# Performance work log

Hardware: AMD Instinct MI355X
Metric: run time of the kernel (lower is better)

The kernel has to match this reference:

```python
import jax, jax.numpy as jnp
import numpy as np

NEG = -1e30  # safe stand-in for -inf in fp32


def _seg_logsumexp(scores, seg, num_segments):
    m = jax.ops.segment_max(scores, seg, num_segments=num_segments)
    m = jnp.maximum(m, NEG)
    s = jax.ops.segment_sum(jnp.exp(scores - m[seg]), seg, num_segments=num_segments)
    return jnp.where(s > 0, m + jnp.log(s), NEG)


def _chain_ll(x, length, src, dst, pdf, logw, init_lp, final_lp):
    # Log-domain HMM forward recursion over an edge-list graph.
    # x: [T, D] log-likelihoods; returns scalar log total path weight.
    S = init_lp.shape[0]
    T = x.shape[0]

    def step(alpha, inputs):
        xt, t = inputs
        scores = alpha[src] + logw + xt[pdf]          # [E]
        new_alpha = _seg_logsumexp(scores, dst, S)    # [S]
        alpha = jnp.where(t < length, new_alpha, alpha)
        return alpha, None

    alpha, _ = jax.lax.scan(step, init_lp, (x, jnp.arange(T)))
    return jax.nn.logsumexp(alpha + final_lp)


def chain_loss(x, x_lengths, den_src, den_dst, den_pdf, den_logw, den_init, den_final,
               num_src, num_dst, num_pdf, num_logw, num_init, num_final):
    # Denominator: one shared graph for all batch elements.
    den_ll = jax.vmap(_chain_ll, in_axes=(0, 0, None, None, None, None, None, None))(
        x, x_lengths, den_src, den_dst, den_pdf, den_logw, den_init, den_final)
    # Numerator: one graph per utterance.
    num_ll = jax.vmap(_chain_ll)(
        x, x_lengths, num_src, num_dst, num_pdf, num_logw, num_init, num_final)
    den_objf = jnp.sum(den_ll)
    num_objf = jnp.sum(num_ll)
    objf = -(num_objf - den_objf)
    return objf / jnp.sum(x_lengths).astype(x.dtype)  # avg=True


def setup_inputs() -> dict:
    key = jax.random.key(0)
    ks = jax.random.split(key, 16)
    B, T, D = 32, 500, 3072
    S_den, E_den = 4000, 120000
    S_num, E_num = 200, 600

    x = jax.random.normal(ks[0], (B, T, D), dtype=jnp.float32)
    x_lengths = jnp.sort(jax.random.randint(ks[1], (B,), T // 2, T + 1, dtype=jnp.int32))[::-1]

    den_src = jax.random.randint(ks[2], (E_den,), 0, S_den, dtype=jnp.int32)
    den_dst = jax.random.randint(ks[3], (E_den,), 0, S_den, dtype=jnp.int32)
    den_pdf = jax.random.randint(ks[4], (E_den,), 0, D, dtype=jnp.int32)
    den_logw = -5.0 * jax.random.uniform(ks[5], (E_den,), dtype=jnp.float32)
    den_init = -3.0 * jax.random.uniform(ks[6], (S_den,), dtype=jnp.float32)
    den_final = -3.0 * jax.random.uniform(ks[7], (S_den,), dtype=jnp.float32)

    num_src = jax.random.randint(ks[8], (B, E_num), 0, S_num, dtype=jnp.int32)
    num_dst = jax.random.randint(ks[9], (B, E_num), 0, S_num, dtype=jnp.int32)
    num_pdf = jax.random.randint(ks[10], (B, E_num), 0, D, dtype=jnp.int32)
    num_logw = -5.0 * jax.random.uniform(ks[11], (B, E_num), dtype=jnp.float32)
    num_init = -3.0 * jax.random.uniform(ks[12], (B, S_num), dtype=jnp.float32)
    num_final = -3.0 * jax.random.uniform(ks[13], (B, S_num), dtype=jnp.float32)

    return {"x": x, "x_lengths": x_lengths,
            "den_src": den_src, "den_dst": den_dst, "den_pdf": den_pdf,
            "den_logw": den_logw, "den_init": den_init, "den_final": den_final,
            "num_src": num_src, "num_dst": num_dst, "num_pdf": num_pdf,
            "num_logw": num_logw, "num_init": num_init, "num_final": num_final}


def reference(x, x_lengths, den_src, den_dst, den_pdf, den_logw, den_init, den_final,
              num_src, num_dst, num_pdf, num_logw, num_init, num_final):
    return chain_loss(x, x_lengths, den_src, den_dst, den_pdf, den_logw, den_init, den_final,
                      num_src, num_dst, num_pdf, num_logw, num_init, num_final)
```

## Files before the change

### kernel.cpp

```cpp
#include <hip/hip_runtime.h>

constexpr int B_     = 32;
constexpr int T_     = 500;
constexpr int D_     = 3072;
constexpr int S_DEN  = 4000;
constexpr int E_DEN  = 120000;
constexpr int S_NUM  = 200;
constexpr int E_NUM  = 600;
constexpr int NCHUNK = 8;
constexpr int WTGT   = (E_DEN + 2 * E_NUM) / NCHUNK;
constexpr int ECAP   = 15488;
constexpr int NTB    = 512;

__global__ void zero_ints(int* p, int n) {
    int i = blockIdx.x * 256 + threadIdx.x;
    if (i < n) p[i] = 0;
}

__global__ void hist_den(const int* __restrict__ dst, int* __restrict__ cnt) {
    int e = blockIdx.x * 256 + threadIdx.x;
    if (e < E_DEN) atomicAdd(&cnt[dst[e]], 1);
}

__global__ void hist_num(const int* __restrict__ dst, int* __restrict__ cnt) {
    int b = blockIdx.y, j = blockIdx.x * 256 + threadIdx.x;
    if (j < E_NUM) atomicAdd(&cnt[b * S_NUM + dst[b * E_NUM + j]], 1);
}

__global__ void scan_den(int* __restrict__ cnt_cur, int* __restrict__ row) {
    __shared__ int part[1024];
    int tid = threadIdx.x, base = tid * 4;
    int c[4], pre[4], s = 0;
    #pragma unroll
    for (int j = 0; j < 4; ++j) {
        int idx = base + j;
        c[j] = (idx < S_DEN) ? cnt_cur[idx] : 0;
        pre[j] = s; s += c[j];
    }
    part[tid] = s; __syncthreads();
    for (int off = 1; off < 1024; off <<= 1) {
        int v = (tid >= off) ? part[tid - off] : 0; __syncthreads();
        part[tid] += v; __syncthreads();
    }
    int offs = (tid > 0) ? part[tid - 1] : 0;
    #pragma unroll
    for (int j = 0; j < 4; ++j) {
        int idx = base + j;
        if (idx < S_DEN) { row[idx] = offs + pre[j]; cnt_cur[idx] = offs + pre[j]; }
    }
    if (tid == 1023) row[S_DEN] = part[1023];
}

__global__ void scan_num(int* __restrict__ cnt_cur, int* __restrict__ row) {
    __shared__ int part[256];
    int b = blockIdx.x, tid = threadIdx.x;
    int c = (tid < S_NUM) ? cnt_cur[b * S_NUM + tid] : 0;
    part[tid] = c; __syncthreads();
    for (int off = 1; off < 256; off <<= 1) {
        int v = (tid >= off) ? part[tid - off] : 0; __syncthreads();
        part[tid] += v; __syncthreads();
    }
    int excl = part[tid] - c;
    if (tid < S_NUM) { row[b * (S_NUM + 1) + tid] = excl; cnt_cur[b * S_NUM + tid] = excl; }
    if (tid == 255) row[b * (S_NUM + 1) + S_NUM] = part[255];
}

__global__ void scatter_den(const int* __restrict__ src, const int* __restrict__ dst,
                            const int* __restrict__ pdf, const float* __restrict__ logw,
                            int* __restrict__ cur, int2* __restrict__ csr) {
    int e = blockIdx.x * 256 + threadIdx.x;
    if (e >= E_DEN) return;
    int pos = atomicAdd(&cur[dst[e]], 1);
    csr[pos] = make_int2(src[e] | (pdf[e] << 12), __float_as_int(__expf(logw[e])));
}

__global__ void scatter_num(const int* __restrict__ src, const int* __restrict__ dst,
                            const int* __restrict__ pdf, const float* __restrict__ logw,
                            int* __restrict__ cur, int2* __restrict__ csr) {
    int b = blockIdx.y, j = blockIdx.x * 256 + threadIdx.x;
    if (j >= E_NUM) return;
    int e = b * E_NUM + j;
    int pos = atomicAdd(&cur[b * S_NUM + dst[e]], 1);
    csr[b * E_NUM + pos] = make_int2(src[e] | (pdf[e] << 12), __float_as_int(__expf(logw[e])));
}

__global__ void part_den(const int* __restrict__ row, int* __restrict__ part) {
    int r = threadIdx.x;
    if (r > NCHUNK) return;
    if (r == 0)        { part[0] = 0; return; }
    if (r == NCHUNK)   { part[NCHUNK] = S_DEN; return; }
    int target = r * WTGT; if (target > E_DEN) target = E_DEN;
    int lo = 0, hi = S_DEN;
    while (lo < hi) { int mid = (lo + hi) >> 1; if (row[mid] < target) lo = mid + 1; else hi = mid; }
    part[r] = lo;
}

__global__ __launch_bounds__(NTB, 1)
void chain_persist(const float* __restrict__ x, const int* __restrict__ x_lengths,
                   const int* __restrict__ den_row, const int2* __restrict__ den_csr,
                   const int* __restrict__ part,
                   const int* __restrict__ num_row, const int2* __restrict__ num_csr,
                   const float* __restrict__ den_init, const float* __restrict__ den_final,
                   const float* __restrict__ num_init, const float* __restrict__ num_final,
                   unsigned long long* __restrict__ EAslot,
                   unsigned long long* __restrict__ Fflag,
                   float* __restrict__ ll) {
    __shared__ int2   csr_d[ECAP];
    __shared__ float4 ex4[D_ / 4];
    __shared__ float  eal[S_DEN];
    __shared__ int2   csr_n[E_NUM];
    __shared__ float  eal_n[S_NUM];
    __shared__ float  red[8], red_n[8];
    float* ex = (float*)ex4;

    const int tid = threadIdx.x;
    const int b   = blockIdx.x & 31;
    const int r   = blockIdx.x >> 5;
    const int len = x_lengths[b];

    const int s0 = part[r], s1 = part[r + 1];
    const int e0 = den_row[s0], e1 = den_row[s1];
    const int ne = e1 - e0;
    for (int i = tid; i < ne; i += NTB) csr_d[i] = den_csr[e0 + i];
    const int sa = s0 + tid, sb = s0 + tid + NTB;
    int ba = 0, eaA = 0, bb = 0, ebB = 0;
    if (sa < s1) { ba = den_row[sa] - e0; eaA = den_row[sa + 1] - e0; }
    if (sb < s1) { bb = den_row[sb] - e0; ebB = den_row[sb + 1] - e0; }
    for (int s = tid; s < S_DEN; s += NTB) eal[s] = __expf(den_init[s]);

    int nb = 0, neE = 0;
    if (r == NCHUNK - 1) {
        for (int i = tid; i < E_NUM; i += NTB) csr_n[i] = num_csr[b * E_NUM + i];
        if (tid < S_NUM) {
            nb  = num_row[b * (S_NUM + 1) + tid];
            neE = num_row[b * (S_NUM + 1) + tid + 1];
            eal_n[tid] = __expf(num_init[b * S_NUM + tid]);
        }
    }

    const float* xb = x + (size_t)b * T_ * D_;
    const bool  has2 = tid < (D_ / 4 - NTB);
    float4 xr0, xr1;
    {
        const float4* p = (const float4*)xb;
        xr0 = p[tid];
        xr1 = has2 ? p[tid + NTB] : make_float4(0.f, 0.f, 0.f, 0.f);
        float4 ev;
        ev.x = __expf(fminf(xr0.x, 60.f)); ev.y = __expf(fminf(xr0.y, 60.f));
        ev.z = __expf(fminf(xr0.z, 60.f)); ev.w = __expf(fminf(xr0.w, 60.f));
        ex4[tid] = ev;
        if (has2) {
            float4 e1v;
            e1v.x = __expf(fminf(xr1.x, 60.f)); e1v.y = __expf(fminf(xr1.y, 60.f));
            e1v.z = __expf(fminf(xr1.z, 60.f)); e1v.w = __expf(fminf(xr1.w, 60.f));
            ex4[tid + NTB] = e1v;
        }
        if (len > 1) {
            const float4* pn = (const float4*)(xb + (size_t)D_);
            xr0 = pn[tid];
            if (has2) xr1 = pn[tid + NTB];
        }
    }
    __syncthreads();

    float off = 0.f, offn = 0.f, acc0 = 0.f, acc1 = 0.f, accn = 0.f;
    float inv_prev = 1.f;

    for (int t = 0; t < len; ++t) {
        float raw0 = 0.f, raw1 = 0.f;
        if (sa < s1) {
            float a0 = 0.f, a1 = 0.f;
            int e = ba;
            for (; e + 2 <= eaA; e += 2) {
                int2 p0 = csr_d[e], p1 = csr_d[e + 1];
                a0 += eal[p0.x & 0xFFF] * __int_as_float(p0.y) * ex[p0.x >> 12];
                a1 += eal[p1.x & 0xFFF] * __int_as_float(p1.y) * ex[p1.x >> 12];
            }
            if (e < eaA) {
                int2 p0 = csr_d[e];
                a0 += eal[p0.x & 0xFFF] * __int_as_float(p0.y) * ex[p0.x >> 12];
            }
            raw0 = a0 + a1;
        }
        if (sb < s1) {
            float a0 = 0.f, a1 = 0.f;
            int e = bb;
            for (; e + 2 <= ebB; e += 2) {
                int2 p0 = csr_d[e], p1 = csr_d[e + 1];
                a0 += eal[p0.x & 0xFFF] * __int_as_float(p0.y) * ex[p0.x >> 12];
                a1 += eal[p1.x & 0xFFF] * __int_as_float(p1.y) * ex[p1.x >> 12];
            }
            if (e < ebB) {
                int2 p0 = csr_d[e];
                a0 += eal[p0.x & 0xFFF] * __int_as_float(p0.y) * ex[p0.x >> 12];
            }
            raw1 = a0 + a1;
        }
        acc0 = raw0 * inv_prev;
        acc1 = raw1 * inv_prev;

        if (t + 1 < len) {
            unsigned long long* slw = EAslot + ((size_t)(t & 1) * B_ + b) * S_DEN;
            const unsigned long long tg = (unsigned long long)(unsigned)(t + 1) << 32;
            if (sa < s1)
                __hip_atomic_store(&slw[sa], tg | __float_as_uint(acc0),
                                   __ATOMIC_RELAXED, __HIP_MEMORY_SCOPE_AGENT);
            if (sb < s1)
                __hip_atomic_store(&slw[sb], tg | __float_as_uint(acc1),
                                   __ATOMIC_RELAXED, __HIP_MEMORY_SCOPE_AGENT);
        }

        float lmax_n = 0.f;
        if (r == NCHUNK - 1) {
            if (tid < S_NUM) {
                float a = 0.f;
                for (int e = nb; e < neE; ++e) {
                    int2 p0 = csr_n[e];
                    a += eal_n[p0.x & 0xFFF] * __int_as_float(p0.y) * ex[p0.x >> 12];
                }
                accn = a; lmax_n = a;
            }
            #pragma unroll
            for (int o = 32; o > 0; o >>= 1) lmax_n = fmaxf(lmax_n, __shfl_down(lmax_n, o));
            if ((tid & 63) == 0) red_n[tid >> 6] = lmax_n;
        }
        __syncthreads();

        if (r == NCHUNK - 1) {
            float Mn = red_n[0];
            #pragma unroll
            for (int w = 1; w < 8; ++w) Mn = fmaxf(Mn, red_n[w]);
            if (!(Mn > 0.f)) Mn = 1.f;
            if (tid < S_NUM) eal_n[tid] = accn / Mn;
            offn += __logf(Mn);
        }

        if (t + 1 < len) {
            float4 ev;
            ev.x = __expf(fminf(xr0.x, 60.f)); ev.y = __expf(fminf(xr0.y, 60.f));
            ev.z = __expf(fminf(xr0.z, 60.f)); ev.w = __expf(fminf(xr0.w, 60.f));
            ex4[tid] = ev;
            if (has2) {
                float4 e1v;
                e1v.x = __expf(fminf(xr1.x, 60.f)); e1v.y = __expf(fminf(xr1.y, 60.f));
                e1v.z = __expf(fminf(xr1.z, 60.f)); e1v.w = __expf(fminf(xr1.w, 60.f));
                ex4[tid + NTB] = e1v;
            }
            if (t + 2 < len) {
                const float4* pn = (const float4*)(xb + (size_t)(t + 2) * D_);
                xr0 = pn[tid];
                if (has2) xr1 = pn[tid + NTB];
            }

            const unsigned long long* slr = EAslot + ((size_t)(t & 1) * B_ + b) * S_DEN;
            const unsigned want = (unsigned)(t + 1);
            float mv = 0.f;
            unsigned rdy = 0;
            while (rdy != 0xFFu) {
                #pragma unroll
                for (int k = 0; k < 8; ++k) {
                    if (rdy & (1u << k)) continue;
                    int s = tid + k * NTB;
                    if (s >= S_DEN) { rdy |= 1u << k; continue; }
                    unsigned long long v = __hip_atomic_load(&slr[s],
                                             __ATOMIC_RELAXED, __HIP_MEMORY_SCOPE_AGENT);
                    if ((unsigned)(v >> 32) == want) {
                        float f = __uint_as_float((unsigned)v);
                        eal[s] = f;
                        mv = fmaxf(mv, f);
                        rdy |= 1u << k;
                    }
                }
                if (rdy != 0xFFu) __builtin_amdgcn_s_sleep(1);
            }
            #pragma unroll
            for (int o = 32; o > 0; o >>= 1) mv = fmaxf(mv, __shfl_down(mv, o));
            if ((tid & 63) == 0) red[tid >> 6] = mv;
            __syncthreads();

            float M = red[0];
            #pragma unroll
            for (int w = 1; w < 8; ++w) M = fmaxf(M, red[w]);
            if (!(M > 0.f)) M = 1.f;
            off += __logf(M);
            inv_prev = 1.f / M;
        }
    }

    float fs = 0.f;
    if (sa < s1) fs += acc0 * __expf(den_final[sa]);
    if (sb < s1) fs += acc1 * __expf(den_final[sb]);
    #pragma unroll
    for (int o = 32; o > 0; o >>= 1) fs += __shfl_down(fs, o);
    if ((tid & 63) == 0) red[tid >> 6] = fs;
    __syncthreads();

    if (tid == 0) {
        float bf = 0.f;
        #pragma unroll
        for (int w = 0; w < 8; ++w) bf += red[w];
        unsigned long long pv = ((unsigned long long)(unsigned)len << 32) |
                                (unsigned long long)__float_as_uint(bf);
        __hip_atomic_store(&Fflag[b * 8 + r], pv, __ATOMIC_RELAXED, __HIP_MEMORY_SCOPE_AGENT);
    }

    if (r == 0 && tid < 64) {
        float sv = 0.f;
        bool rdy = (tid >= 8);
        const unsigned want = (unsigned)len;
        while (true) {
            if (!rdy) {
                unsigned long long v = __hip_atomic_load(&Fflag[b * 8 + tid],
                                         __ATOMIC_RELAXED, __HIP_MEMORY_SCOPE_AGENT);
                if ((unsigned)(v >> 32) == want) { rdy = true; sv = __uint_as_float((unsigned)v); }
            }
            if (__all(rdy)) break;
            __builtin_amdgcn_s_sleep(1);
        }
        #pragma unroll
        for (int o = 4; o > 0; o >>= 1) sv += __shfl_down(sv, o);
        if (tid == 0) ll[b] = __logf(sv) + off;
    }

    if (r == NCHUNK - 1) {
        float ns = (tid < S_NUM) ? eal_n[tid] * __expf(num_final[b * S_NUM + tid]) : 0.f;
        #pragma unroll
        for (int o = 32; o > 0; o >>= 1) ns += __shfl_down(ns, o);
        if ((tid & 63) == 0) red_n[tid >> 6] = ns;
        __syncthreads();
        if (tid == 0) {
            float tn = 0.f;
            #pragma unroll
            for (int w = 0; w < 8; ++w) tn += red_n[w];
            ll[B_ + b] = __logf(tn) + offn;
        }
    }
}

__global__ void finalize_loss(const float* __restrict__ ll, const int* __restrict__ x_lengths,
                              float* __restrict__ out) {
    int tid = threadIdx.x;
    float d = (tid < B_) ? ll[tid] : 0.f;
    float n = (tid < B_) ? ll[B_ + tid] : 0.f;
    float l = (tid < B_) ? (float)x_lengths[tid] : 0.f;
    #pragma unroll
    for (int o = 32; o > 0; o >>= 1) {
        d += __shfl_down(d, o); n += __shfl_down(n, o); l += __shfl_down(l, o);
    }
    if (tid == 0) out[0] = (d - n) / l;
}

__global__ __launch_bounds__(1024)
void chain_forward_atomic(const float* __restrict__ x, const int* __restrict__ x_lengths,
                          const int* __restrict__ den_src, const int* __restrict__ den_dst,
                          const int* __restrict__ den_pdf, const float* __restrict__ den_logw,
                          const float* __restrict__ den_init, const float* __restrict__ den_final,
                          const int* __restrict__ num_src, const int* __restrict__ num_dst,
                          const int* __restrict__ num_pdf, const float* __restrict__ num_logw,
                          const float* __restrict__ num_init, const float* __restrict__ num_final,
                          float* __restrict__ ll_out) {
    __shared__ float ea[S_DEN];
    __shared__ float ssum[S_DEN];
    __shared__ float ex[D_];
    __shared__ float red[16];
    __shared__ float s_m;
    const int  tid = threadIdx.x;
    const bool is_den = blockIdx.x < B_;
    const int  b = is_den ? blockIdx.x : blockIdx.x - B_;
    const int  S = is_den ? S_DEN : S_NUM;
    const int  E = is_den ? E_DEN : E_NUM;
    const int*   esrc = is_den ? den_src : num_src + b * E_NUM;
    const int*   edst = is_den ? den_dst : num_dst + b * E_NUM;
    const int*   epdf = is_den ? den_pdf : num_pdf + b * E_NUM;
    const float* elw  = is_den ? den_logw: num_logw + b * E_NUM;
    const float* init = is_den ? den_init : num_init + b * S_NUM;
    const float* fin  = is_den ? den_final: num_final + b * S_NUM;
    const int    len  = x_lengths[b];
    const float* xb   = x + (size_t)b * T_ * D_;
    for (int s = tid; s < S; s += 1024) { ea[s] = __expf(init[s]); ssum[s] = 0.f; }
    float off = 0.f;
    for (int t = 0; t < len; ++t) {
        const float4* xr4 = reinterpret_cast<const float4*>(xb + (size_t)t * D_);
        for (int d = tid; d < D_ / 4; d += 1024) {
            float4 v = xr4[d];
            ex[4*d+0] = __expf(fminf(v.x, 60.f)); ex[4*d+1] = __expf(fminf(v.y, 60.f));
            ex[4*d+2] = __expf(fminf(v.z, 60.f)); ex[4*d+3] = __expf(fminf(v.w, 60.f));
        }
        __syncthreads();
        for (int e = tid; e < E; e += 1024)
            unsafeAtomicAdd(&ssum[edst[e]], ea[esrc[e]] * __expf(elw[e]) * ex[epdf[e]]);
        __syncthreads();
        float lm = 0.f;
        for (int s = tid; s < S; s += 1024) lm = fmaxf(lm, ssum[s]);
        #pragma unroll
        for (int o = 32; o > 0; o >>= 1) lm = fmaxf(lm, __shfl_down(lm, o));
        if ((tid & 63) == 0) red[tid >> 6] = lm;
        __syncthreads();
        if (tid == 0) {
            float m = red[0];
            for (int w = 1; w < 16; ++w) m = fmaxf(m, red[w]);
            s_m = (m > 0.f) ? m : 1.f;
        }
        __syncthreads();
        float inv = 1.f / s_m;
        off += __logf(s_m);
        for (int s = tid; s < S; s += 1024) { ea[s] = ssum[s] * inv; ssum[s] = 0.f; }
    }
    float lsum = 0.f;
    for (int s = tid; s < S; s += 1024) lsum += ea[s] * __expf(fin[s]);
    #pragma unroll
    for (int o = 32; o > 0; o >>= 1) lsum += __shfl_down(lsum, o);
    if ((tid & 63) == 0) red[tid >> 6] = lsum;
    __syncthreads();
    if (tid == 0) {
        float tot = 0.f;
        for (int w = 0; w < 16; ++w) tot += red[w];
        ll_out[blockIdx.x] = off + __logf(tot);
    }
}

static inline size_t align16(size_t v) { return (v + 15) & ~size_t(15); }

extern "C" void kernel_launch(void* const* d_in, const int* in_sizes, int n_in,
                              void* d_out, int out_size, void* d_ws, size_t ws_size,
                              hipStream_t stream) {
    const float* x         = (const float*)d_in[0];
    const int*   x_lengths = (const int*)  d_in[1];
    const int*   den_src   = (const int*)  d_in[2];
    const int*   den_dst   = (const int*)  d_in[3];
    const int*   den_pdf   = (const int*)  d_in[4];
    const float* den_logw  = (const float*)d_in[5];
    const float* den_init  = (const float*)d_in[6];
    const float* den_final = (const float*)d_in[7];
    const int*   num_src   = (const int*)  d_in[8];
    const int*   num_dst   = (const int*)  d_in[9];
    const int*   num_pdf   = (const int*)  d_in[10];
    const float* num_logw  = (const float*)d_in[11];
    const float* num_init  = (const float*)d_in[12];
    const float* num_final = (const float*)d_in[13];

    char* ws = (char*)d_ws;
    size_t o = 0;
    float*              ll      = (float*)             (ws + o); o = align16(o + 64 * sizeof(float));
    int*                den_row = (int*)               (ws + o); o = align16(o + (S_DEN + 1) * sizeof(int));
    int*                den_cur = (int*)               (ws + o); o = align16(o + S_DEN * sizeof(int));
    int*                num_row = (int*)               (ws + o); o = align16(o + B_ * (S_NUM + 1) * sizeof(int));
    int*                num_cur = (int*)               (ws + o); o = align16(o + B_ * S_NUM * sizeof(int));
    int2*               den_csr = (int2*)              (ws + o); o = align16(o + (size_t)E_DEN * sizeof(int2));
    int2*               num_csr = (int2*)              (ws + o); o = align16(o + (size_t)B_ * E_NUM * sizeof(int2));
    int*                part    = (int*)               (ws + o); o = align16(o + (NCHUNK + 1) * sizeof(int));
    unsigned long long* EAslot  = (unsigned long long*)(ws + o); o = align16(o + (size_t)2 * B_ * S_DEN * sizeof(unsigned long long));
    unsigned long long* Fflag   = (unsigned long long*)(ws + o); o = align16(o + (size_t)B_ * 8 * sizeof(unsigned long long));
    const size_t need = o;

    if (ws_size >= need) {
        zero_ints<<<(S_DEN + 255) / 256, 256, 0, stream>>>(den_cur, S_DEN);
        zero_ints<<<(B_ * S_NUM + 255) / 256, 256, 0, stream>>>(num_cur, B_ * S_NUM);
        hist_den<<<(E_DEN + 255) / 256, 256, 0, stream>>>(den_dst, den_cur);
        hist_num<<<dim3(3, B_), 256, 0, stream>>>(num_dst, num_cur);
        scan_den<<<1, 1024, 0, stream>>>(den_cur, den_row);
        scan_num<<<B_, 256, 0, stream>>>(num_cur, num_row);
        scatter_den<<<(E_DEN + 255) / 256, 256, 0, stream>>>(
            den_src, den_dst, den_pdf, den_logw, den_cur, den_csr);
        scatter_num<<<dim3(3, B_), 256, 0, stream>>>(
            num_src, num_dst, num_pdf, num_logw, num_cur, num_csr);
        part_den<<<1, 16, 0, stream>>>(den_row, part);

        void* args[] = {
            (void*)&x, (void*)&x_lengths, (void*)&den_row, (void*)&den_csr, (void*)&part,
            (void*)&num_row, (void*)&num_csr, (void*)&den_init, (void*)&den_final,
            (void*)&num_init, (void*)&num_final, (void*)&EAslot,
            (void*)&Fflag, (void*)&ll
        };
        hipError_t err = hipLaunchCooperativeKernel((const void*)chain_persist,
                                                    dim3(B_ * NCHUNK), dim3(NTB),
                                                    args, 0, stream);
        if (err != hipSuccess) {
            chain_persist<<<dim3(B_ * NCHUNK), dim3(NTB), 0, stream>>>(
                x, x_lengths, den_row, den_csr, part, num_row, num_csr,
                den_init, den_final, num_init, num_final,
                EAslot, Fflag, ll);
        }
        finalize_loss<<<1, 64, 0, stream>>>(ll, x_lengths, (float*)d_out);
    } else {
        chain_forward_atomic<<<2 * B_, 1024, 0, stream>>>(
            x, x_lengths, den_src, den_dst, den_pdf, den_logw, den_init, den_final,
            num_src, num_dst, num_pdf, num_logw, num_init, num_final, ll);
        finalize_loss<<<1, 64, 0, stream>>>(ll, x_lengths, (float*)d_out);
    }
}
```

Baseline: 3.385 ms.

## Group CSR edges by source chunk to overlap cross-block waits with compute

Edges of each destination state are now sorted into sub-ranges keyed by which chunk owns the source state, using an extra histogram, scan and grouped scatter. Each time step first processes edges whose sources are local, then waits for each remote chunk's published alpha values in turn and processes those edges as they arrive. This hides inter-block synchronization latency behind useful work instead of waiting for all 4000 states before computing. Slot values are also prefetched right after publishing. The cost is more per-step __syncthreads, extra register arrays, and the normalization max is now applied only after all partial sums are in.

```diff
diff --git a/kernel.cpp b/kernel.cpp
--- a/kernel.cpp
+++ b/kernel.cpp
@@ -65,25 +65,6 @@
     if (tid == 255) row[b * (S_NUM + 1) + S_NUM] = part[255];
 }
 
-__global__ void scatter_den(const int* __restrict__ src, const int* __restrict__ dst,
-                            const int* __restrict__ pdf, const float* __restrict__ logw,
-                            int* __restrict__ cur, int2* __restrict__ csr) {
-    int e = blockIdx.x * 256 + threadIdx.x;
-    if (e >= E_DEN) return;
-    int pos = atomicAdd(&cur[dst[e]], 1);
-    csr[pos] = make_int2(src[e] | (pdf[e] << 12), __float_as_int(__expf(logw[e])));
-}
-
-__global__ void scatter_num(const int* __restrict__ src, const int* __restrict__ dst,
-                            const int* __restrict__ pdf, const float* __restrict__ logw,
-                            int* __restrict__ cur, int2* __restrict__ csr) {
-    int b = blockIdx.y, j = blockIdx.x * 256 + threadIdx.x;
-    if (j >= E_NUM) return;
-    int e = b * E_NUM + j;
-    int pos = atomicAdd(&cur[b * S_NUM + dst[e]], 1);
-    csr[b * E_NUM + pos] = make_int2(src[e] | (pdf[e] << 12), __float_as_int(__expf(logw[e])));
-}
-
 __global__ void part_den(const int* __restrict__ row, int* __restrict__ part) {
     int r = threadIdx.x;
     if (r > NCHUNK) return;
@@ -95,10 +76,57 @@
     part[r] = lo;
 }
 
+__global__ void hist2_den(const int* __restrict__ src, const int* __restrict__ dst,
+                          const int* __restrict__ part, int* __restrict__ cnt2) {
+    int e = blockIdx.x * 256 + threadIdx.x;
+    if (e >= E_DEN) return;
+    int s = src[e], g = 0;
+    #pragma unroll
+    for (int k = 1; k < NCHUNK; ++k) g += (s >= part[k]);
+    atomicAdd(&cnt2[dst[e] * NCHUNK + g], 1);
+}
+
+__global__ void scan2_den(const int* __restrict__ den_row, int* __restrict__ cnt2,
+                          int* __restrict__ rgb) {
+    int s = blockIdx.x * 256 + threadIdx.x;
+    if (s >= S_DEN) return;
+    int acc = den_row[s];
+    #pragma unroll
+    for (int g = 0; g < NCHUNK; ++g) {
+        int c = cnt2[s * NCHUNK + g];
+        rgb[s * NCHUNK + g] = acc;
+        cnt2[s * NCHUNK + g] = acc;
+        acc += c;
+    }
+}
+
+__global__ void scatter_den_grp(const int* __restrict__ src, const int* __restrict__ dst,
+                                const int* __restrict__ pdf, const float* __restrict__ logw,
+                                const int* __restrict__ part, int* __restrict__ cur2,
+                                int2* __restrict__ csr) {
+    int e = blockIdx.x * 256 + threadIdx.x;
+    if (e >= E_DEN) return;
+    int s = src[e], g = 0;
+    #pragma unroll
+    for (int k = 1; k < NCHUNK; ++k) g += (s >= part[k]);
+    int pos = atomicAdd(&cur2[dst[e] * NCHUNK + g], 1);
+    csr[pos] = make_int2(s | (pdf[e] << 12), __float_as_int(__expf(logw[e])));
+}
+
+__global__ void scatter_num(const int* __restrict__ src, const int* __restrict__ dst,
+                            const int* __restrict__ pdf, const float* __restrict__ logw,
+                            int* __restrict__ cur, int2* __restrict__ csr) {
+    int b = blockIdx.y, j = blockIdx.x * 256 + threadIdx.x;
+    if (j >= E_NUM) return;
+    int e = b * E_NUM + j;
+    int pos = atomicAdd(&cur[b * S_NUM + dst[e]], 1);
+    csr[b * E_NUM + pos] = make_int2(src[e] | (pdf[e] << 12), __float_as_int(__expf(logw[e])));
+}
+
 __global__ __launch_bounds__(NTB, 1)
 void chain_persist(const float* __restrict__ x, const int* __restrict__ x_lengths,
                    const int* __restrict__ den_row, const int2* __restrict__ den_csr,
-                   const int* __restrict__ part,
+                   const int* __restrict__ part, const int* __restrict__ rgb,
                    const int* __restrict__ num_row, const int2* __restrict__ num_csr,
                    const float* __restrict__ den_init, const float* __restrict__ den_final,
                    const float* __restrict__ num_init, const float* __restrict__ num_final,
@@ -118,14 +146,28 @@
     const int r   = blockIdx.x >> 5;
     const int len = x_lengths[b];
 
-    const int s0 = part[r], s1 = part[r + 1];
+    int pg[NCHUNK + 1];
+    #pragma unroll
+    for (int i = 0; i <= NCHUNK; ++i) pg[i] = part[i];
+
+    const int s0 = pg[r], s1 = pg[r + 1];
     const int e0 = den_row[s0], e1 = den_row[s1];
     const int ne = e1 - e0;
     for (int i = tid; i < ne; i += NTB) csr_d[i] = den_csr[e0 + i];
     const int sa = s0 + tid, sb = s0 + tid + NTB;
-    int ba = 0, eaA = 0, bb = 0, ebB = 0;
-    if (sa < s1) { ba = den_row[sa] - e0; eaA = den_row[sa + 1] - e0; }
-    if (sb < s1) { bb = den_row[sb] - e0; ebB = den_row[sb + 1] - e0; }
+    int rb0[NCHUNK + 1], rb1[NCHUNK + 1];
+    #pragma unroll
+    for (int g = 0; g <= NCHUNK; ++g) { rb0[g] = 0; rb1[g] = 0; }
+    if (sa < s1) {
+        #pragma unroll
+        for (int g = 0; g < NCHUNK; ++g) rb0[g] = rgb[sa * NCHUNK + g] - e0;
+        rb0[NCHUNK] = den_row[sa + 1] - e0;
+    }
+    if (sb < s1) {
+        #pragma unroll
+        for (int g = 0; g < NCHUNK; ++g) rb1[g] = rgb[sb * NCHUNK + g] - e0;
+        rb1[NCHUNK] = den_row[sb + 1] - e0;
+    }
     for (int s = tid; s < S_DEN; s += NTB) eal[s] = __expf(den_init[s]);
 
     int nb = 0, neE = 0;
@@ -163,41 +205,147 @@
     }
     __syncthreads();
 
-    float off = 0.f, offn = 0.f, acc0 = 0.f, acc1 = 0.f, accn = 0.f;
-    float inv_prev = 1.f;
-
-    for (int t = 0; t < len; ++t) {
+#define PROC_ROW(ebeg, eend, raw) do {                                          \
+        int e_ = (ebeg), en_ = (eend);                                          \
+        float a0_ = 0.f, a1_ = 0.f;                                             \
+        for (; e_ + 2 <= en_; e_ += 2) {                                        \
+            int2 p0_ = csr_d[e_], p1_ = csr_d[e_ + 1];                          \
+            a0_ += eal[p0_.x & 0xFFF] * __int_as_float(p0_.y) * ex[p0_.x >> 12];\
+            a1_ += eal[p1_.x & 0xFFF] * __int_as_float(p1_.y) * ex[p1_.x >> 12];\
+        }                                                                       \
+        if (e_ < en_) {                                                         \
+            int2 p0_ = csr_d[e_];                                               \
+            a0_ += eal[p0_.x & 0xFFF] * __int_as_float(p0_.y) * ex[p0_.x >> 12];\
+        }                                                                       \
+        raw += a0_ + a1_;                                                       \
+    } while (0)
+
+    float off = 0.f, offn = 0.f;
+    float acc0 = 0.f, acc1 = 0.f, accn = 0.f;
+    unsigned long long pfA[NCHUNK - 1], pfB[NCHUNK - 1];
+
+    {
         float raw0 = 0.f, raw1 = 0.f;
-        if (sa < s1) {
-            float a0 = 0.f, a1 = 0.f;
-            int e = ba;
-            for (; e + 2 <= eaA; e += 2) {
-                int2 p0 = csr_d[e], p1 = csr_d[e + 1];
-                a0 += eal[p0.x & 0xFFF] * __int_as_float(p0.y) * ex[p0.x >> 12];
-                a1 += eal[p1.x & 0xFFF] * __int_as_float(p1.y) * ex[p1.x >> 12];
-            }
-            if (e < eaA) {
-                int2 p0 = csr_d[e];
-                a0 += eal[p0.x & 0xFFF] * __int_as_float(p0.y) * ex[p0.x >> 12];
-            }
-            raw0 = a0 + a1;
-        }
-        if (sb < s1) {
-            float a0 = 0.f, a1 = 0.f;
-            int e = bb;
-            for (; e + 2 <= ebB; e += 2) {
-                int2 p0 = csr_d[e], p1 = csr_d[e + 1];
-                a0 += eal[p0.x & 0xFFF] * __int_as_float(p0.y) * ex[p0.x >> 12];
-                a1 += eal[p1.x & 0xFFF] * __int_as_float(p1.y) * ex[p1.x >> 12];
-            }
-            if (e < ebB) {
-                int2 p0 = csr_d[e];
-                a0 += eal[p0.x & 0xFFF] * __int_as_float(p0.y) * ex[p0.x >> 12];
-            }
-            raw1 = a0 + a1;
-        }
-        acc0 = raw0 * inv_prev;
-        acc1 = raw1 * inv_prev;
+        if (sa < s1) PROC_ROW(rb0[0], rb0[NCHUNK], raw0);
+        if (sb < s1) PROC_ROW(rb1[0], rb1[NCHUNK], raw1);
+        acc0 = raw0; acc1 = raw1;
+
+        if (len > 1) {
+            unsigned long long* slw = EAslot + ((size_t)0 * B_ + b) * S_DEN;
+            const unsigned long long tg = 1ull << 32;
+            if (sa < s1)
+                __hip_atomic_store(&slw[sa], tg | __float_as_uint(acc0),
+                                   __ATOMIC_RELAXED, __HIP_MEMORY_SCOPE_AGENT);
+            if (sb < s1)
+                __hip_atomic_store(&slw[sb], tg | __float_as_uint(acc1),
+                                   __ATOMIC_RELAXED, __HIP_MEMORY_SCOPE_AGENT);
+            #pragma unroll
+            for (int i = 1; i < NCHUNK; ++i) {
+                int gg = (r + i) & 7;
+                int s = pg[gg] + tid, s2 = s + NTB;
+                pfA[i-1] = (s  < pg[gg+1]) ? __hip_atomic_load(&slw[s],  __ATOMIC_RELAXED, __HIP_MEMORY_SCOPE_AGENT) : 0ull;
+                pfB[i-1] = (s2 < pg[gg+1]) ? __hip_atomic_load(&slw[s2], __ATOMIC_RELAXED, __HIP_MEMORY_SCOPE_AGENT) : 0ull;
+            }
+        }
+        if (r == NCHUNK - 1) {
+            float lmax_n = 0.f;
+            if (tid < S_NUM) {
+                float a = 0.f;
+                for (int e = nb; e < neE; ++e) {
+                    int2 p0 = csr_n[e];
+                    a += eal_n[p0.x & 0xFFF] * __int_as_float(p0.y) * ex[p0.x >> 12];
+                }
+                accn = a; lmax_n = a;
+            }
+            #pragma unroll
+            for (int o = 32; o > 0; o >>= 1) lmax_n = fmaxf(lmax_n, __shfl_down(lmax_n, o));
+            if ((tid & 63) == 0) red_n[tid >> 6] = lmax_n;
+            __syncthreads();
+            float Mn = red_n[0];
+            #pragma unroll
+            for (int w = 1; w < 8; ++w) Mn = fmaxf(Mn, red_n[w]);
+            if (!(Mn > 0.f)) Mn = 1.f;
+            if (tid < S_NUM) eal_n[tid] = accn / Mn;
+            offn += __logf(Mn);
+        }
+    }
+
+    for (int t = 1; t < len; ++t) {
+        __syncthreads();
+
+        {
+            float4 ev;
+            ev.x = __expf(fminf(xr0.x, 60.f)); ev.y = __expf(fminf(xr0.y, 60.f));
+            ev.z = __expf(fminf(xr0.z, 60.f)); ev.w = __expf(fminf(xr0.w, 60.f));
+            ex4[tid] = ev;
+            if (has2) {
+                float4 e1v;
+                e1v.x = __expf(fminf(xr1.x, 60.f)); e1v.y = __expf(fminf(xr1.y, 60.f));
+                e1v.z = __expf(fminf(xr1.z, 60.f)); e1v.w = __expf(fminf(xr1.w, 60.f));
+                ex4[tid + NTB] = e1v;
+            }
+            if (t + 1 < len) {
+                const float4* pn = (const float4*)(xb + (size_t)(t + 1) * D_);
+                xr0 = pn[tid];
+                if (has2) xr1 = pn[tid + NTB];
+            }
+        }
+        float mv = 0.f;
+        if (sa < s1) { eal[sa] = acc0; mv = acc0; }
+        if (sb < s1) { eal[sb] = acc1; mv = fmaxf(mv, acc1); }
+        __syncthreads();
+
+        float raw0 = 0.f, raw1 = 0.f;
+        if (sa < s1) PROC_ROW(rb0[r], rb0[r + 1], raw0);
+        if (sb < s1) PROC_ROW(rb1[r], rb1[r + 1], raw1);
+
+        const unsigned long long* slr = EAslot + ((size_t)((t - 1) & 1) * B_ + b) * S_DEN;
+        const unsigned want = (unsigned)t;
+        float inv = 1.f;
+
+        #pragma unroll
+        for (int i = 1; i < NCHUNK; ++i) {
+            const int gg = (r + i) & 7;
+            int s = pg[gg] + tid;
+            if (s < pg[gg + 1]) {
+                unsigned long long v = pfA[i-1];
+                while ((unsigned)(v >> 32) != want) {
+                    __builtin_amdgcn_s_sleep(1);
+                    v = __hip_atomic_load(&slr[s], __ATOMIC_RELAXED, __HIP_MEMORY_SCOPE_AGENT);
+                }
+                float f = __uint_as_float((unsigned)v);
+                eal[s] = f; mv = fmaxf(mv, f);
+                int s2 = s + NTB;
+                if (s2 < pg[gg + 1]) {
+                    v = pfB[i-1];
+                    while ((unsigned)(v >> 32) != want) {
+                        __builtin_amdgcn_s_sleep(1);
+                        v = __hip_atomic_load(&slr[s2], __ATOMIC_RELAXED, __HIP_MEMORY_SCOPE_AGENT);
+                    }
+                    f = __uint_as_float((unsigned)v);
+                    eal[s2] = f; mv = fmaxf(mv, f);
+                }
+            }
+            if (i == NCHUNK - 1) {
+                #pragma unroll
+                for (int o = 32; o > 0; o >>= 1) mv = fmaxf(mv, __shfl_down(mv, o));
+                if ((tid & 63) == 0) red[tid >> 6] = mv;
+            }
+            __syncthreads();
+            if (i == NCHUNK - 1) {
+                float M = red[0];
+                #pragma unroll
+                for (int w = 1; w < 8; ++w) M = fmaxf(M, red[w]);
+                if (!(M > 0.f)) M = 1.f;
+                inv = 1.f / M;
+                off += __logf(M);
+            }
+            if (sa < s1) PROC_ROW(rb0[gg], rb0[gg + 1], raw0);
+            if (sb < s1) PROC_ROW(rb1[gg], rb1[gg + 1], raw1);
+        }
+
+        acc0 = raw0 * inv;
+        acc1 = raw1 * inv;
 
         if (t + 1 < len) {
             unsigned long long* slw = EAslot + ((size_t)(t & 1) * B_ + b) * S_DEN;
@@ -208,10 +356,17 @@
             if (sb < s1)
                 __hip_atomic_store(&slw[sb], tg | __float_as_uint(acc1),
                                    __ATOMIC_RELAXED, __HIP_MEMORY_SCOPE_AGENT);
-        }
-
-        float lmax_n = 0.f;
+            #pragma unroll
+            for (int i = 1; i < NCHUNK; ++i) {
+                int gg = (r + i) & 7;
+                int s = pg[gg] + tid, s2 = s + NTB;
+                pfA[i-1] = (s  < pg[gg+1]) ? __hip_atomic_load(&slw[s],  __ATOMIC_RELAXED, __HIP_MEMORY_SCOPE_AGENT) : 0ull;
+                pfB[i-1] = (s2 < pg[gg+1]) ? __hip_atomic_load(&slw[s2], __ATOMIC_RELAXED, __HIP_MEMORY_SCOPE_AGENT) : 0ull;
+            }
+        }
+
         if (r == NCHUNK - 1) {
+            float lmax_n = 0.f;
             if (tid < S_NUM) {
                 float a = 0.f;
                 for (int e = nb; e < neE; ++e) {
@@ -223,10 +378,7 @@
             #pragma unroll
             for (int o = 32; o > 0; o >>= 1) lmax_n = fmaxf(lmax_n, __shfl_down(lmax_n, o));
             if ((tid & 63) == 0) red_n[tid >> 6] = lmax_n;
-        }
-        __syncthreads();
-
-        if (r == NCHUNK - 1) {
+            __syncthreads();
             float Mn = red_n[0];
             #pragma unroll
             for (int w = 1; w < 8; ++w) Mn = fmaxf(Mn, red_n[w]);
@@ -234,58 +386,8 @@
             if (tid < S_NUM) eal_n[tid] = accn / Mn;
             offn += __logf(Mn);
         }
-
-        if (t + 1 < len) {
-            float4 ev;
-            ev.x = __expf(fminf(xr0.x, 60.f)); ev.y = __expf(fminf(xr0.y, 60.f));
-            ev.z = __expf(fminf(xr0.z, 60.f)); ev.w = __expf(fminf(xr0.w, 60.f));
-            ex4[tid] = ev;
-            if (has2) {
-                float4 e1v;
-                e1v.x = __expf(fminf(xr1.x, 60.f)); e1v.y = __expf(fminf(xr1.y, 60.f));
-                e1v.z = __expf(fminf(xr1.z, 60.f)); e1v.w = __expf(fminf(xr1.w, 60.f));
-                ex4[tid + NTB] = e1v;
-            }
-            if (t + 2 < len) {
-                const float4* pn = (const float4*)(xb + (size_t)(t + 2) * D_);
-                xr0 = pn[tid];
-                if (has2) xr1 = pn[tid + NTB];
-            }
-
-            const unsigned long long* slr = EAslot + ((size_t)(t & 1) * B_ + b) * S_DEN;
-            const unsigned want = (unsigned)(t + 1);
-            float mv = 0.f;
-            unsigned rdy = 0;
-            while (rdy != 0xFFu) {
-                #pragma unroll
-                for (int k = 0; k < 8; ++k) {
-                    if (rdy & (1u << k)) continue;
-                    int s = tid + k * NTB;
-                    if (s >= S_DEN) { rdy |= 1u << k; continue; }
-                    unsigned long long v = __hip_atomic_load(&slr[s],
-                                             __ATOMIC_RELAXED, __HIP_MEMORY_SCOPE_AGENT);
-                    if ((unsigned)(v >> 32) == want) {
-                        float f = __uint_as_float((unsigned)v);
-                        eal[s] = f;
-                        mv = fmaxf(mv, f);
-                        rdy |= 1u << k;
-                    }
-                }
-                if (rdy != 0xFFu) __builtin_amdgcn_s_sleep(1);
-            }
-            #pragma unroll
-            for (int o = 32; o > 0; o >>= 1) mv = fmaxf(mv, __shfl_down(mv, o));
-            if ((tid & 63) == 0) red[tid >> 6] = mv;
-            __syncthreads();
-
-            float M = red[0];
-            #pragma unroll
-            for (int w = 1; w < 8; ++w) M = fmaxf(M, red[w]);
-            if (!(M > 0.f)) M = 1.f;
-            off += __logf(M);
-            inv_prev = 1.f / M;
-        }
-    }
+    }
+#undef PROC_ROW
 
     float fs = 0.f;
     if (sa < s1) fs += acc0 * __expf(den_final[sa]);
@@ -449,6 +551,8 @@
     int2*               den_csr = (int2*)              (ws + o); o = align16(o + (size_t)E_DEN * sizeof(int2));
     int2*               num_csr = (int2*)              (ws + o); o = align16(o + (size_t)B_ * E_NUM * sizeof(int2));
     int*                part    = (int*)               (ws + o); o = align16(o + (NCHUNK + 1) * sizeof(int));
+    int*                cnt2    = (int*)               (ws + o); o = align16(o + (size_t)S_DEN * NCHUNK * sizeof(int));
+    int*                rgb     = (int*)               (ws + o); o = align16(o + (size_t)S_DEN * NCHUNK * sizeof(int));
     unsigned long long* EAslot  = (unsigned long long*)(ws + o); o = align16(o + (size_t)2 * B_ * S_DEN * sizeof(unsigned long long));
     unsigned long long* Fflag   = (unsigned long long*)(ws + o); o = align16(o + (size_t)B_ * 8 * sizeof(unsigned long long));
     const size_t need = o;
@@ -456,28 +560,30 @@
     if (ws_size >= need) {
         zero_ints<<<(S_DEN + 255) / 256, 256, 0, stream>>>(den_cur, S_DEN);
         zero_ints<<<(B_ * S_NUM + 255) / 256, 256, 0, stream>>>(num_cur, B_ * S_NUM);
+        zero_ints<<<(S_DEN * NCHUNK + 255) / 256, 256, 0, stream>>>(cnt2, S_DEN * NCHUNK);
         hist_den<<<(E_DEN + 255) / 256, 256, 0, stream>>>(den_dst, den_cur);
         hist_num<<<dim3(3, B_), 256, 0, stream>>>(num_dst, num_cur);
         scan_den<<<1, 1024, 0, stream>>>(den_cur, den_row);
         scan_num<<<B_, 256, 0, stream>>>(num_cur, num_row);
-        scatter_den<<<(E_DEN + 255) / 256, 256, 0, stream>>>(
-            den_src, den_dst, den_pdf, den_logw, den_cur, den_csr);
+        part_den<<<1, 16, 0, stream>>>(den_row, part);
+        hist2_den<<<(E_DEN + 255) / 256, 256, 0, stream>>>(den_src, den_dst, part, cnt2);
+        scan2_den<<<(S_DEN + 255) / 256, 256, 0, stream>>>(den_row, cnt2, rgb);
+        scatter_den_grp<<<(E_DEN + 255) / 256, 256, 0, stream>>>(
+            den_src, den_dst, den_pdf, den_logw, part, cnt2, den_csr);
         scatter_num<<<dim3(3, B_), 256, 0, stream>>>(
             num_src, num_dst, num_pdf, num_logw, num_cur, num_csr);
-        part_den<<<1, 16, 0, stream>>>(den_row, part);
 
         void* args[] = {
             (void*)&x, (void*)&x_lengths, (void*)&den_row, (void*)&den_csr, (void*)&part,
-            (void*)&num_row, (void*)&num_csr, (void*)&den_init, (void*)&den_final,
-            (void*)&num_init, (void*)&num_final, (void*)&EAslot,
-            (void*)&Fflag, (void*)&ll
+            (void*)&rgb, (void*)&num_row, (void*)&num_csr, (void*)&den_init, (void*)&den_final,
+            (void*)&num_init, (void*)&num_final, (void*)&EAslot, (void*)&Fflag, (void*)&ll
         };
         hipError_t err = hipLaunchCooperativeKernel((const void*)chain_persist,
                                                     dim3(B_ * NCHUNK), dim3(NTB),
                                                     args, 0, stream);
         if (err != hipSuccess) {
             chain_persist<<<dim3(B_ * NCHUNK), dim3(NTB), 0, stream>>>(
-                x, x_lengths, den_row, den_csr, part, num_row, num_csr,
+                x, x_lengths, den_row, den_csr, part, rgb, num_row, num_csr,
                 den_init, den_final, num_init, num_final,
                 EAslot, Fflag, ll);
         }
```

New measurement: 4.496 ms. 32.8% more time.

## Store alpha and emission tables as duplicated fp16 in LDS

Applied to the files above, without the earlier changes.

Converts the shared-memory emission (exp x) and forward-alpha tables from fp32 to fp16. Each table is stored twice, and threads pick a copy by lane parity, which is meant to reduce LDS bank conflicts on the random gathers in the edge loop. Alpha values are pre-scaled by 1/256 to stay in fp16 range, and the emission exponent clamp is tightened from 60 to 10. This cuts LDS footprint and may improve gather throughput, at the cost of fp16 precision and clamping of large log-likelihoods, which changes results for inputs above 10.

```diff
diff --git a/kernel.cpp b/kernel.cpp
--- a/kernel.cpp
+++ b/kernel.cpp
@@ -1,4 +1,5 @@
 #include <hip/hip_runtime.h>
+#include <hip/hip_fp16.h>
 
 constexpr int B_     = 32;
 constexpr int T_     = 500;
@@ -12,6 +13,9 @@
 constexpr int ECAP   = 15488;
 constexpr int NTB    = 512;
 
+#define SCL  0.00390625f
+#define ISCL 256.0f
+
 __global__ void zero_ints(int* p, int n) {
     int i = blockIdx.x * 256 + threadIdx.x;
     if (i < n) p[i] = 0;
@@ -106,17 +110,18 @@
                    unsigned long long* __restrict__ Fflag,
                    float* __restrict__ ll) {
     __shared__ int2   csr_d[ECAP];
-    __shared__ float4 ex4[D_ / 4];
-    __shared__ float  eal[S_DEN];
+    __shared__ __half exh[2][D_];
+    __shared__ __half ealh[2][S_DEN];
     __shared__ int2   csr_n[E_NUM];
     __shared__ float  eal_n[S_NUM];
     __shared__ float  red[8], red_n[8];
-    float* ex = (float*)ex4;
 
     const int tid = threadIdx.x;
     const int b   = blockIdx.x & 31;
     const int r   = blockIdx.x >> 5;
     const int len = x_lengths[b];
+    const __half* myeal = ealh[tid & 1];
+    const __half* myex  = exh[tid & 1];
 
     const int s0 = part[r], s1 = part[r + 1];
     const int e0 = den_row[s0], e1 = den_row[s1];
@@ -126,7 +131,10 @@
     int ba = 0, eaA = 0, bb = 0, ebB = 0;
     if (sa < s1) { ba = den_row[sa] - e0; eaA = den_row[sa + 1] - e0; }
     if (sb < s1) { bb = den_row[sb] - e0; ebB = den_row[sb + 1] - e0; }
-    for (int s = tid; s < S_DEN; s += NTB) eal[s] = __expf(den_init[s]);
+    for (int s = tid; s < S_DEN; s += NTB) {
+        __half h = __float2half_rn(__expf(den_init[s]) * SCL);
+        ealh[0][s] = h; ealh[1][s] = h;
+    }
 
     int nb = 0, neE = 0;
     if (r == NCHUNK - 1) {
@@ -141,20 +149,25 @@
     const float* xb = x + (size_t)b * T_ * D_;
     const bool  has2 = tid < (D_ / 4 - NTB);
     float4 xr0, xr1;
+
+#define STAGE_EX(vreg, base_d) do {                                            \
+        __half2 h01_, h23_;                                                    \
+        h01_.x = __float2half_rn(__expf(fminf((vreg).x, 10.f)));               \
+        h01_.y = __float2half_rn(__expf(fminf((vreg).y, 10.f)));               \
+        h23_.x = __float2half_rn(__expf(fminf((vreg).z, 10.f)));               \
+        h23_.y = __float2half_rn(__expf(fminf((vreg).w, 10.f)));               \
+        ((__half2*)&exh[0][0])[2*(base_d)]     = h01_;                         \
+        ((__half2*)&exh[0][0])[2*(base_d) + 1] = h23_;                         \
+        ((__half2*)&exh[1][0])[2*(base_d)]     = h01_;                         \
+        ((__half2*)&exh[1][0])[2*(base_d) + 1] = h23_;                         \
+    } while (0)
+
     {
         const float4* p = (const float4*)xb;
         xr0 = p[tid];
         xr1 = has2 ? p[tid + NTB] : make_float4(0.f, 0.f, 0.f, 0.f);
-        float4 ev;
-        ev.x = __expf(fminf(xr0.x, 60.f)); ev.y = __expf(fminf(xr0.y, 60.f));
-        ev.z = __expf(fminf(xr0.z, 60.f)); ev.w = __expf(fminf(xr0.w, 60.f));
-        ex4[tid] = ev;
-        if (has2) {
-            float4 e1v;
-            e1v.x = __expf(fminf(xr1.x, 60.f)); e1v.y = __expf(fminf(xr1.y, 60.f));
-            e1v.z = __expf(fminf(xr1.z, 60.f)); e1v.w = __expf(fminf(xr1.w, 60.f));
-            ex4[tid + NTB] = e1v;
-        }
+        STAGE_EX(xr0, tid);
+        if (has2) STAGE_EX(xr1, tid + NTB);
         if (len > 1) {
             const float4* pn = (const float4*)(xb + (size_t)D_);
             xr0 = pn[tid];
@@ -163,39 +176,31 @@
     }
     __syncthreads();
 
+#define PROC_ROW(ebeg, eend, raw) do {                                          \
+        int e_ = (ebeg), en_ = (eend);                                          \
+        float a0_ = 0.f, a1_ = 0.f;                                             \
+        for (; e_ + 2 <= en_; e_ += 2) {                                        \
+            int2 p0_ = csr_d[e_], p1_ = csr_d[e_ + 1];                          \
+            a0_ += __half2float(myeal[p0_.x & 0xFFF]) * __int_as_float(p0_.y)   \
+                   * __half2float(myex[p0_.x >> 12]);                           \
+            a1_ += __half2float(myeal[p1_.x & 0xFFF]) * __int_as_float(p1_.y)   \
+                   * __half2float(myex[p1_.x >> 12]);                           \
+        }                                                                       \
+        if (e_ < en_) {                                                         \
+            int2 p0_ = csr_d[e_];                                               \
+            a0_ += __half2float(myeal[p0_.x & 0xFFF]) * __int_as_float(p0_.y)   \
+                   * __half2float(myex[p0_.x >> 12]);                           \
+        }                                                                       \
+        raw += a0_ + a1_;                                                       \
+    } while (0)
+
     float off = 0.f, offn = 0.f, acc0 = 0.f, acc1 = 0.f, accn = 0.f;
-    float inv_prev = 1.f;
+    float inv_prev = ISCL;
 
     for (int t = 0; t < len; ++t) {
         float raw0 = 0.f, raw1 = 0.f;
-        if (sa < s1) {
-            float a0 = 0.f, a1 = 0.f;
-            int e = ba;
-            for (; e + 2 <= eaA; e += 2) {
-                int2 p0 = csr_d[e], p1 = csr_d[e + 1];
-                a0 += eal[p0.x & 0xFFF] * __int_as_float(p0.y) * ex[p0.x >> 12];
-                a1 += eal[p1.x & 0xFFF] * __int_as_float(p1.y) * ex[p1.x >> 12];
-            }
-            if (e < eaA) {
-                int2 p0 = csr_d[e];
-                a0 += eal[p0.x & 0xFFF] * __int_as_float(p0.y) * ex[p0.x >> 12];
-            }
-            raw0 = a0 + a1;
-        }
-        if (sb < s1) {
-            float a0 = 0.f, a1 = 0.f;
-            int e = bb;
-            for (; e + 2 <= ebB; e += 2) {
-                int2 p0 = csr_d[e], p1 = csr_d[e + 1];
-                a0 += eal[p0.x & 0xFFF] * __int_as_float(p0.y) * ex[p0.x >> 12];
-                a1 += eal[p1.x & 0xFFF] * __int_as_float(p1.y) * ex[p1.x >> 12];
-            }
-            if (e < ebB) {
-                int2 p0 = csr_d[e];
-                a0 += eal[p0.x & 0xFFF] * __int_as_float(p0.y) * ex[p0.x >> 12];
-            }
-            raw1 = a0 + a1;
-        }
+        if (sa < s1) PROC_ROW(ba, eaA, raw0);
+        if (sb < s1) PROC_ROW(bb, ebB, raw1);
         acc0 = raw0 * inv_prev;
         acc1 = raw1 * inv_prev;
 
@@ -216,7 +221,8 @@
                 float a = 0.f;
                 for (int e = nb; e < neE; ++e) {
                     int2 p0 = csr_n[e];
-                    a += eal_n[p0.x & 0xFFF] * __int_as_float(p0.y) * ex[p0.x >> 12];
+                    a += eal_n[p0.x & 0xFFF] * __int_as_float(p0.y)
+                         * __half2float(myex[p0.x >> 12]);
                 }
                 accn = a; lmax_n = a;
             }
@@ -236,16 +242,8 @@
         }
 
         if (t + 1 < len) {
-            float4 ev;
-            ev.x = __expf(fminf(xr0.x, 60.f)); ev.y = __expf(fminf(xr0.y, 60.f));
-            ev.z = __expf(fminf(xr0.z, 60.f)); ev.w = __expf(fminf(xr0.w, 60.f));
-            ex4[tid] = ev;
-            if (has2) {
-                float4 e1v;
-                e1v.x = __expf(fminf(xr1.x, 60.f)); e1v.y = __expf(fminf(xr1.y, 60.f));
-                e1v.z = __expf(fminf(xr1.z, 60.f)); e1v.w = __expf(fminf(xr1.w, 60.f));
-                ex4[tid + NTB] = e1v;
-            }
+            STAGE_EX(xr0, tid);
+            if (has2) STAGE_EX(xr1, tid + NTB);
             if (t + 2 < len) {
                 const float4* pn = (const float4*)(xb + (size_t)(t + 2) * D_);
                 xr0 = pn[tid];
@@ -266,7 +264,8 @@
                                              __ATOMIC_RELAXED, __HIP_MEMORY_SCOPE_AGENT);
                     if ((unsigned)(v >> 32) == want) {
                         float f = __uint_as_float((unsigned)v);
-                        eal[s] = f;
+                        __half h = __float2half_rn(f * SCL);
+                        ealh[0][s] = h; ealh[1][s] = h;
                         mv = fmaxf(mv, f);
                         rdy |= 1u << k;
                     }
@@ -283,9 +282,11 @@
             for (int w = 1; w < 8; ++w) M = fmaxf(M, red[w]);
             if (!(M > 0.f)) M = 1.f;
             off += __logf(M);
-            inv_prev = 1.f / M;
-        }
-    }
+            inv_prev = ISCL / M;
+        }
+    }
+#undef PROC_ROW
+#undef STAGE_EX
 
     float fs = 0.f;
     if (sa < s1) fs += acc0 * __expf(den_final[sa]);
```

After: 3.488 ms. +3.1%, slower.
